# Optimization experiments

Hardware: AMD Instinct MI355X
Metric: run time of the kernel (lower is better)

Reference implementation:

```python
import jax, jax.numpy as jnp
import numpy as np

B, S, E = 4, 2048, 1024
H = 16
D = E // H  # head_dim = 64


def setup_inputs() -> dict:
    key = jax.random.key(0)
    ks = jax.random.split(key, 7)
    query = jax.random.normal(ks[0], (B, S, E), dtype=jnp.float32)
    k_in = jax.random.normal(ks[1], (B, S, E), dtype=jnp.float32)
    v_in = jax.random.normal(ks[2], (B, S, E), dtype=jnp.float32)
    lim_qkv = 1.0 / np.sqrt(E)
    W_qkv = jax.random.uniform(ks[3], (E, 3 * E), jnp.float32, -lim_qkv, lim_qkv)
    b_qkv = jax.random.uniform(ks[4], (3 * E,), jnp.float32, -lim_qkv, lim_qkv)
    W_out = jax.random.uniform(ks[5], (E, E), jnp.float32, -lim_qkv, lim_qkv)
    b_out = jax.random.uniform(ks[6], (E,), jnp.float32, -lim_qkv, lim_qkv)
    return {"query": query, "key": k_in, "value": v_in,
            "W_qkv": W_qkv, "b_qkv": b_qkv, "W_out": W_out, "b_out": b_out}


def reference(query, key, value, W_qkv, b_qkv, W_out, b_out):
    # NOTE: original module ignores key/value; q,k,v all derived from query.
    b, s, e = query.shape
    qkv = query @ W_qkv + b_qkv                     # [B,S,3E]
    qkv = qkv.reshape(b, s, 3, H, D)
    q, k, v = qkv[:, :, 0], qkv[:, :, 1], qkv[:, :, 2]   # [B,S,H,D]
    scale = jnp.sqrt(jnp.asarray(D, dtype=jnp.float32))
    scores = jnp.einsum('bqhd,bkhd->bhqk', q, k) / scale  # [B,H,S,S]
    attn = jax.nn.softmax(scores, axis=-1)
    out = jnp.einsum('bhqk,bkhd->bqhd', attn, v).reshape(b, s, e)
    return out @ W_out + b_out
```

## Files before the change

### kernel.cpp

```cpp
#include <hip/hip_runtime.h>
#include <hip/hip_bf16.h>

#define Bc 4
#define Sc 2048
#define Ec 1024
#define Hc 16
#define Dc 64

typedef __bf16 bf16_t;
typedef __bf16 bf16x8 __attribute__((ext_vector_type(8)));
typedef float f32x4 __attribute__((ext_vector_type(4)));

extern "C" __device__ float __ocml_native_exp2_f32(float);

__device__ __forceinline__ f32x4 mfma16(bf16x8 a, bf16x8 b, f32x4 c) {
    return __builtin_amdgcn_mfma_f32_16x16x32_bf16(a, b, c, 0, 0, 0);
}

__device__ __forceinline__ void gload16(const bf16_t* g, bf16_t* l) {
    __builtin_amdgcn_global_load_lds(
        (const __attribute__((address_space(1))) unsigned int*)g,
        (__attribute__((address_space(3))) unsigned int*)l, 16, 0, 0);
}

__global__ __launch_bounds__(256)
void cvt_bf16(const float* __restrict__ in, bf16_t* __restrict__ out, int n4)
{
    int i = blockIdx.x * 256 + threadIdx.x;
    if (i >= n4) return;
    float4 v = ((const float4*)in)[i];
    alignas(8) bf16_t o[4];
    o[0] = (bf16_t)v.x; o[1] = (bf16_t)v.y; o[2] = (bf16_t)v.z; o[3] = (bf16_t)v.w;
    ((uint2*)out)[i] = *(uint2*)o;
}

__global__ __launch_bounds__(256)
void transpose_w(const float* __restrict__ W, bf16_t* __restrict__ Wt, int K, int N)
{
    __shared__ float T[64][65];
    const int kt = blockIdx.y, nt = blockIdx.x;
    const int r = threadIdx.x >> 4;
    const int c = (threadIdx.x & 15) * 4;
    #pragma unroll
    for (int p = 0; p < 4; p++) {
        float4 v = *(const float4*)(W + (size_t)(kt*64 + r + p*16)*N + nt*64 + c);
        T[r + p*16][c] = v.x; T[r + p*16][c+1] = v.y;
        T[r + p*16][c+2] = v.z; T[r + p*16][c+3] = v.w;
    }
    __syncthreads();
    #pragma unroll
    for (int p = 0; p < 4; p++) {
        int n = nt*64 + r + p*16;
        alignas(8) bf16_t tmp[4];
        #pragma unroll
        for (int j = 0; j < 4; j++) tmp[j] = (bf16_t)T[c + j][r + p*16];
        *(uint2*)(Wt + (size_t)n*K + kt*64 + c) = *(uint2*)tmp;
    }
}

__global__ __launch_bounds__(256)
void transpose_v(const bf16_t* __restrict__ qkv, bf16_t* __restrict__ vt)
{
    __shared__ bf16_t T[64][72];
    const int bh = blockIdx.y, st = blockIdx.x;
    const int b = bh >> 4, h = bh & 15;
    const int sr = threadIdx.x >> 3;
    const int dc = (threadIdx.x & 7) * 8;
    #pragma unroll
    for (int p = 0; p < 2; p++) {
        const bf16_t* src = qkv + (size_t)(b*Sc + st*64 + sr + p*32)*(3*Ec) + 2*Ec + h*Dc + dc;
        *(uint4*)&T[sr + p*32][dc] = *(const uint4*)src;
    }
    __syncthreads();
    const int dr = threadIdx.x >> 3;
    const int sc2 = (threadIdx.x & 7) * 8;
    #pragma unroll
    for (int p = 0; p < 2; p++) {
        alignas(16) bf16_t tmp[8];
        #pragma unroll
        for (int j = 0; j < 8; j++) {
            int q = sc2 + j;
            int o = ((q & 3) << 4) | (q >> 2);
            tmp[j] = T[o][dr + p*32];
        }
        *(uint4*)(vt + (size_t)bh*Dc*Sc + (size_t)(dr + p*32)*Sc + st*64 + sc2) = *(uint4*)tmp;
    }
}

template<int OUT_IS_F32>
__global__ __launch_bounds__(256)
void gemm_bt(const bf16_t* __restrict__ A, const bf16_t* __restrict__ Bt,
             const float* __restrict__ biasp, void* __restrict__ Cp,
             int M, int N, int K)
{
    __shared__ bf16_t As[2][128*32];
    __shared__ bf16_t Bs[2][128*32];

    const int tid  = threadIdx.x;
    const int wave = tid >> 6;
    const int lane = tid & 63;
    const int quad = lane >> 4;
    const int l16  = lane & 15;
    const int wm   = (wave >> 1) * 64;
    const int wn   = (wave & 1) * 64;
    const int m0   = blockIdx.y * 128;
    const int n0   = blockIdx.x * 128;

    const int srow = wave*32 + (lane >> 2);
    const int scol = (lane & 3) * 8;
    const bf16_t* ap0 = A  + (size_t)(m0 + srow)      * K + scol;
    const bf16_t* ap1 = A  + (size_t)(m0 + srow + 16) * K + scol;
    const bf16_t* bp0 = Bt + (size_t)(n0 + srow)      * K + scol;
    const bf16_t* bp1 = Bt + (size_t)(n0 + srow + 16) * K + scol;
    bf16_t* asl0 = &As[0][(wave*32)      * 32];
    bf16_t* asl1 = &As[0][(wave*32 + 16) * 32];
    bf16_t* bsl0 = &Bs[0][(wave*32)      * 32];
    bf16_t* bsl1 = &Bs[0][(wave*32 + 16) * 32];
    bf16_t* asl2 = &As[1][(wave*32)      * 32];
    bf16_t* asl3 = &As[1][(wave*32 + 16) * 32];
    bf16_t* bsl2 = &Bs[1][(wave*32)      * 32];
    bf16_t* bsl3 = &Bs[1][(wave*32 + 16) * 32];

    f32x4 acc[4][4] = {};

    for (int k0 = 0; k0 < K; k0 += 64) {
        gload16(ap0 + k0,      asl0);
        gload16(ap1 + k0,      asl1);
        gload16(ap0 + k0 + 32, asl2);
        gload16(ap1 + k0 + 32, asl3);
        gload16(bp0 + k0,      bsl0);
        gload16(bp1 + k0,      bsl1);
        gload16(bp0 + k0 + 32, bsl2);
        gload16(bp1 + k0 + 32, bsl3);
        __syncthreads();

        #pragma unroll
        for (int kc = 0; kc < 2; kc++) {
            bf16x8 af[4], bfr[4];
            #pragma unroll
            for (int mi = 0; mi < 4; mi++)
                af[mi] = *(const bf16x8*)&As[kc][(wm + mi*16 + l16)*32 + quad*8];
            #pragma unroll
            for (int ni = 0; ni < 4; ni++)
                bfr[ni] = *(const bf16x8*)&Bs[kc][(wn + ni*16 + l16)*32 + quad*8];
            #pragma unroll
            for (int mi = 0; mi < 4; mi++)
                #pragma unroll
                for (int ni = 0; ni < 4; ni++)
                    acc[mi][ni] = mfma16(af[mi], bfr[ni], acc[mi][ni]);
        }
        __syncthreads();
    }

    float bv[4];
    #pragma unroll
    for (int ni = 0; ni < 4; ni++) bv[ni] = biasp[n0 + wn + ni*16 + l16];

    #pragma unroll
    for (int mi = 0; mi < 4; mi++)
        #pragma unroll
        for (int ni = 0; ni < 4; ni++)
            #pragma unroll
            for (int r = 0; r < 4; r++) {
                int row = m0 + wm + mi*16 + quad*4 + r;
                int col = n0 + wn + ni*16 + l16;
                float v = acc[mi][ni][r] + bv[ni];
                if (OUT_IS_F32) ((float*)Cp)[(size_t)row * N + col] = v;
                else            ((bf16_t*)Cp)[(size_t)row * N + col] = (bf16_t)v;
            }
}

__global__ __launch_bounds__(256, 2)
void attn5(const bf16_t* __restrict__ qkv, const bf16_t* __restrict__ vt,
           bf16_t* __restrict__ aout)
{
    __shared__ bf16_t Ks[64][72];
    __shared__ bf16_t Vs[64][72];
    __shared__ bf16_t Ps[4][64][72];

    const int tid  = threadIdx.x;
    const int wave = tid >> 6;
    const int lane = tid & 63;
    const int quad = lane >> 4;
    const int l16  = lane & 15;
    const int bh   = blockIdx.y;
    const int b    = bh >> 4;
    const int h    = bh & 15;
    const int qt   = blockIdx.x;
    const float kscale = 0.125f * 1.44269504088896340736f;

    bf16x8 qf[4][2];
    #pragma unroll
    for (int mi = 0; mi < 4; mi++) {
        const bf16_t* qrow = qkv + (size_t)(b*Sc + qt*256 + wave*64 + mi*16 + l16)*(3*Ec) + h*Dc;
        qf[mi][0] = *(const bf16x8*)(qrow + quad*8);
        qf[mi][1] = *(const bf16x8*)(qrow + 32 + quad*8);
        #pragma unroll
        for (int f = 0; f < 2; f++)
            #pragma unroll
            for (int e = 0; e < 8; e++)
                qf[mi][f][e] = (bf16_t)((float)qf[mi][f][e] * kscale);
    }

    bf16x8 ones;
    #pragma unroll
    for (int e = 0; e < 8; e++) ones[e] = (bf16_t)1.0f;

    f32x4 acc[4][4] = {};
    f32x4 acc_l[4] = {};

    const int krw   = tid >> 2;
    const int dbase = (tid & 3) * 16;

    const bf16_t* kbase = qkv + (size_t)(b*Sc + krw)*(3*Ec) + Ec + h*Dc + dbase;
    const bf16_t* vbase = vt + (size_t)bh*Dc*Sc + (size_t)krw*Sc + dbase;
    const size_t kstep = (size_t)64 * (3*Ec);
    uint4 ku0 = ((const uint4*)kbase)[0];
    uint4 ku1 = ((const uint4*)kbase)[1];
    uint4 vu0 = ((const uint4*)vbase)[0];
    uint4 vu1 = ((const uint4*)vbase)[1];

    for (int kt = 0; kt < Sc/64; kt++) {
        __syncthreads();
        *(uint4*)&Ks[krw][dbase]     = ku0;
        *(uint4*)&Ks[krw][dbase + 8] = ku1;
        *(uint4*)&Vs[krw][dbase]     = vu0;
        *(uint4*)&Vs[krw][dbase + 8] = vu1;
        __syncthreads();

        if (kt < Sc/64 - 1) {
            const bf16_t* kn = kbase + (size_t)(kt+1) * kstep;
            const bf16_t* vn = vbase + (kt+1) * 64;
            ku0 = ((const uint4*)kn)[0];
            ku1 = ((const uint4*)kn)[1];
            vu0 = ((const uint4*)vn)[0];
            vu1 = ((const uint4*)vn)[1];
        }

        bf16x8 kf[4][2];
        #pragma unroll
        for (int ni = 0; ni < 4; ni++) {
            kf[ni][0] = *(const bf16x8*)&Ks[ni*16 + l16][quad*8];
            kf[ni][1] = *(const bf16x8*)&Ks[ni*16 + l16][32 + quad*8];
        }

        #pragma unroll
        for (int mi = 0; mi < 4; mi++) {
            f32x4 sf[4];
            #pragma unroll
            for (int ni = 0; ni < 4; ni++) {
                f32x4 z = {};
                z = mfma16(qf[mi][0], kf[ni][0], z);
                z = mfma16(qf[mi][1], kf[ni][1], z);
                sf[ni] = z;
            }
            #pragma unroll
            for (int rr = 0; rr < 4; rr++) {
                float p0 = __ocml_native_exp2_f32(sf[0][rr]);
                float p1 = __ocml_native_exp2_f32(sf[1][rr]);
                float p2 = __ocml_native_exp2_f32(sf[2][rr]);
                float p3 = __ocml_native_exp2_f32(sf[3][rr]);
                alignas(8) bf16_t pw[4];
                pw[0] = (bf16_t)p0; pw[1] = (bf16_t)p1;
                pw[2] = (bf16_t)p2; pw[3] = (bf16_t)p3;
                *(uint2*)&Ps[wave][mi*16 + quad*4 + rr][4*l16] = *(uint2*)pw;
            }
        }

        asm volatile("s_waitcnt lgkmcnt(0)" ::: "memory");

        bf16x8 pf[4][2];
        #pragma unroll
        for (int mi = 0; mi < 4; mi++) {
            pf[mi][0] = *(const bf16x8*)&Ps[wave][mi*16 + l16][quad*8];
            pf[mi][1] = *(const bf16x8*)&Ps[wave][mi*16 + l16][32 + quad*8];
        }
        #pragma unroll
        for (int mi = 0; mi < 4; mi++) {
            acc_l[mi] = mfma16(pf[mi][0], ones, acc_l[mi]);
            acc_l[mi] = mfma16(pf[mi][1], ones, acc_l[mi]);
        }
        #pragma unroll
        for (int ni = 0; ni < 4; ni++) {
            bf16x8 v0 = *(const bf16x8*)&Vs[ni*16 + l16][quad*8];
            bf16x8 v1 = *(const bf16x8*)&Vs[ni*16 + l16][32 + quad*8];
            #pragma unroll
            for (int mi = 0; mi < 4; mi++) {
                acc[mi][ni] = mfma16(pf[mi][0], v0, acc[mi][ni]);
                acc[mi][ni] = mfma16(pf[mi][1], v1, acc[mi][ni]);
            }
        }
    }

    #pragma unroll
    for (int mi = 0; mi < 4; mi++)
        #pragma unroll
        for (int rr = 0; rr < 4; rr++) {
            float inv = 1.0f / acc_l[mi][rr];
            int row = qt*256 + wave*64 + mi*16 + quad*4 + rr;
            #pragma unroll
            for (int ni = 0; ni < 4; ni++) {
                int col = h*Dc + ni*16 + l16;
                aout[(size_t)(b*Sc + row)*Ec + col] = (bf16_t)(acc[mi][ni][rr] * inv);
            }
        }
}

extern "C" void kernel_launch(void* const* d_in, const int* in_sizes, int n_in,
                              void* d_out, int out_size, void* d_ws, size_t ws_size,
                              hipStream_t stream) {
    const float* query = (const float*)d_in[0];
    const float* W_qkv = (const float*)d_in[3];
    const float* b_qkv = (const float*)d_in[4];
    const float* W_out = (const float*)d_in[5];
    const float* b_out = (const float*)d_in[6];
    float* out = (float*)d_out;

    const size_t MT = (size_t)Bc * Sc;
    char* ws = (char*)d_ws;
    bf16_t* qbf     = (bf16_t*)ws;
    bf16_t* qkv_ws  = (bf16_t*)(ws + MT*Ec*2);
    bf16_t* vt_ws   = (bf16_t*)(ws + MT*Ec*2 + MT*3*Ec*2);
    bf16_t* wqkv_t  = (bf16_t*)(ws + MT*Ec*2 + MT*3*Ec*2 + MT*Ec*2);
    bf16_t* wout_t  = (bf16_t*)(ws + MT*Ec*2 + MT*3*Ec*2 + MT*Ec*2 + (size_t)3*Ec*Ec*2);

    cvt_bf16<<<(MT*Ec/4 + 255)/256, 256, 0, stream>>>(query, qbf, (int)(MT*Ec/4));
    transpose_w<<<dim3(3*Ec/64, Ec/64), 256, 0, stream>>>(W_qkv, wqkv_t, Ec, 3*Ec);
    transpose_w<<<dim3(Ec/64, Ec/64), 256, 0, stream>>>(W_out, wout_t, Ec, Ec);

    gemm_bt<0><<<dim3(3*Ec/128, MT/128), 256, 0, stream>>>(
        qbf, wqkv_t, b_qkv, qkv_ws, (int)MT, 3*Ec, Ec);

    transpose_v<<<dim3(Sc/64, Bc*Hc), 256, 0, stream>>>(qkv_ws, vt_ws);

    attn5<<<dim3(Sc/256, Bc*Hc), 256, 0, stream>>>(qkv_ws, vt_ws, qbf);

    gemm_bt<1><<<dim3(Ec/128, MT/128), 256, 0, stream>>>(
        qbf, wout_t, b_out, out, (int)MT, Ec, Ec);
}
```

Before: 321.4 us.

## Keep softmax probabilities in registers by computing transposed S and O tiles

The attention kernel now computes S^T = K·Q^T so the MFMA output layout of the exp'd scores matches the B-operand layout for the P·V product. This removes the per-wave LDS staging buffer for P and the extra MFMAs that summed row totals against a ones vector. Row sums are accumulated in registers and combined with cross-lane shuffles at the end. Because the output is produced transposed, it is written to a new workspace buffer and a separate transpose kernel restores the [B,S,E] layout, which adds a launch and extra memory traffic. Freeing the LDS lets the launch bound allow three blocks per SM instead of two.

```diff
diff --git a/kernel.cpp b/kernel.cpp
--- a/kernel.cpp
+++ b/kernel.cpp
@@ -8,6 +8,7 @@
 #define Dc 64
 
 typedef __bf16 bf16_t;
+typedef __bf16 bf16x4 __attribute__((ext_vector_type(4)));
 typedef __bf16 bf16x8 __attribute__((ext_vector_type(8)));
 typedef float f32x4 __attribute__((ext_vector_type(4)));
 
@@ -78,12 +79,35 @@
     for (int p = 0; p < 2; p++) {
         alignas(16) bf16_t tmp[8];
         #pragma unroll
-        for (int j = 0; j < 8; j++) {
-            int q = sc2 + j;
-            int o = ((q & 3) << 4) | (q >> 2);
-            tmp[j] = T[o][dr + p*32];
-        }
+        for (int j = 0; j < 8; j++)
+            tmp[j] = T[sc2 + j][dr + p*32];
         *(uint4*)(vt + (size_t)bh*Dc*Sc + (size_t)(dr + p*32)*Sc + st*64 + sc2) = *(uint4*)tmp;
+    }
+}
+
+__global__ __launch_bounds__(256)
+void otransp(const bf16_t* __restrict__ ot, bf16_t* __restrict__ attn)
+{
+    __shared__ bf16_t T[64][72];
+    const int bh = blockIdx.y, st = blockIdx.x;
+    const int b = bh >> 4, h = bh & 15;
+    const int dr = threadIdx.x >> 3;
+    const int sc = (threadIdx.x & 7) * 8;
+    #pragma unroll
+    for (int p = 0; p < 2; p++) {
+        const bf16_t* src = ot + ((size_t)bh*Dc + dr + p*32)*Sc + st*64 + sc;
+        *(uint4*)&T[dr + p*32][sc] = *(const uint4*)src;
+    }
+    __syncthreads();
+    const int sr = threadIdx.x >> 3;
+    const int dc = (threadIdx.x & 7) * 8;
+    #pragma unroll
+    for (int p = 0; p < 2; p++) {
+        alignas(16) bf16_t tmp[8];
+        #pragma unroll
+        for (int j = 0; j < 8; j++)
+            tmp[j] = T[dc + j][sr + p*32];
+        *(uint4*)(attn + (size_t)(b*Sc + st*64 + sr + p*32)*Ec + h*Dc + dc) = *(uint4*)tmp;
     }
 }
 
@@ -170,13 +194,12 @@
             }
 }
 
-__global__ __launch_bounds__(256, 2)
-void attn5(const bf16_t* __restrict__ qkv, const bf16_t* __restrict__ vt,
-           bf16_t* __restrict__ aout)
+__global__ __launch_bounds__(256, 3)
+void attn6(const bf16_t* __restrict__ qkv, const bf16_t* __restrict__ vt,
+           bf16_t* __restrict__ ot)
 {
     __shared__ bf16_t Ks[64][72];
     __shared__ bf16_t Vs[64][72];
-    __shared__ bf16_t Ps[4][64][72];
 
     const int tid  = threadIdx.x;
     const int wave = tid >> 6;
@@ -191,23 +214,19 @@
 
     bf16x8 qf[4][2];
     #pragma unroll
-    for (int mi = 0; mi < 4; mi++) {
-        const bf16_t* qrow = qkv + (size_t)(b*Sc + qt*256 + wave*64 + mi*16 + l16)*(3*Ec) + h*Dc;
-        qf[mi][0] = *(const bf16x8*)(qrow + quad*8);
-        qf[mi][1] = *(const bf16x8*)(qrow + 32 + quad*8);
+    for (int qi = 0; qi < 4; qi++) {
+        const bf16_t* qrow = qkv + (size_t)(b*Sc + qt*256 + wave*64 + qi*16 + l16)*(3*Ec) + h*Dc;
+        qf[qi][0] = *(const bf16x8*)(qrow + quad*8);
+        qf[qi][1] = *(const bf16x8*)(qrow + 32 + quad*8);
         #pragma unroll
         for (int f = 0; f < 2; f++)
             #pragma unroll
             for (int e = 0; e < 8; e++)
-                qf[mi][f][e] = (bf16_t)((float)qf[mi][f][e] * kscale);
-    }
-
-    bf16x8 ones;
-    #pragma unroll
-    for (int e = 0; e < 8; e++) ones[e] = (bf16_t)1.0f;
+                qf[qi][f][e] = (bf16_t)((float)qf[qi][f][e] * kscale);
+    }
 
     f32x4 acc[4][4] = {};
-    f32x4 acc_l[4] = {};
+    float lpart[4] = {};
 
     const int krw   = tid >> 2;
     const int dbase = (tid & 3) * 16;
@@ -239,69 +258,67 @@
 
         bf16x8 kf[4][2];
         #pragma unroll
-        for (int ni = 0; ni < 4; ni++) {
-            kf[ni][0] = *(const bf16x8*)&Ks[ni*16 + l16][quad*8];
-            kf[ni][1] = *(const bf16x8*)&Ks[ni*16 + l16][32 + quad*8];
-        }
-
-        #pragma unroll
-        for (int mi = 0; mi < 4; mi++) {
-            f32x4 sf[4];
-            #pragma unroll
-            for (int ni = 0; ni < 4; ni++) {
+        for (int ki = 0; ki < 4; ki++) {
+            kf[ki][0] = *(const bf16x8*)&Ks[ki*16 + l16][quad*8];
+            kf[ki][1] = *(const bf16x8*)&Ks[ki*16 + l16][32 + quad*8];
+        }
+
+        bf16x4 pp[4][4];
+        #pragma unroll
+        for (int ki = 0; ki < 4; ki++) {
+            #pragma unroll
+            for (int qi = 0; qi < 4; qi++) {
                 f32x4 z = {};
-                z = mfma16(qf[mi][0], kf[ni][0], z);
-                z = mfma16(qf[mi][1], kf[ni][1], z);
-                sf[ni] = z;
+                z = mfma16(kf[ki][0], qf[qi][0], z);
+                z = mfma16(kf[ki][1], qf[qi][1], z);
+                float p0 = __ocml_native_exp2_f32(z[0]);
+                float p1 = __ocml_native_exp2_f32(z[1]);
+                float p2 = __ocml_native_exp2_f32(z[2]);
+                float p3 = __ocml_native_exp2_f32(z[3]);
+                lpart[qi] += (p0 + p1) + (p2 + p3);
+                bf16x4 w;
+                w[0] = (bf16_t)p0; w[1] = (bf16_t)p1;
+                w[2] = (bf16_t)p2; w[3] = (bf16_t)p3;
+                pp[ki][qi] = w;
             }
-            #pragma unroll
-            for (int rr = 0; rr < 4; rr++) {
-                float p0 = __ocml_native_exp2_f32(sf[0][rr]);
-                float p1 = __ocml_native_exp2_f32(sf[1][rr]);
-                float p2 = __ocml_native_exp2_f32(sf[2][rr]);
-                float p3 = __ocml_native_exp2_f32(sf[3][rr]);
-                alignas(8) bf16_t pw[4];
-                pw[0] = (bf16_t)p0; pw[1] = (bf16_t)p1;
-                pw[2] = (bf16_t)p2; pw[3] = (bf16_t)p3;
-                *(uint2*)&Ps[wave][mi*16 + quad*4 + rr][4*l16] = *(uint2*)pw;
+        }
+
+        #pragma unroll
+        for (int c = 0; c < 2; c++) {
+            bf16x8 pcat[4];
+            #pragma unroll
+            for (int qi = 0; qi < 4; qi++)
+                pcat[qi] = __builtin_shufflevector(pp[2*c][qi], pp[2*c+1][qi],
+                                                   0,1,2,3,4,5,6,7);
+            #pragma unroll
+            for (int di = 0; di < 4; di++) {
+                bf16x4 v0 = *(const bf16x4*)&Vs[di*16 + l16][c*32 + 4*quad];
+                bf16x4 v1 = *(const bf16x4*)&Vs[di*16 + l16][c*32 + 16 + 4*quad];
+                bf16x8 vf = __builtin_shufflevector(v0, v1, 0,1,2,3,4,5,6,7);
+                #pragma unroll
+                for (int qi = 0; qi < 4; qi++)
+                    acc[di][qi] = mfma16(vf, pcat[qi], acc[di][qi]);
             }
         }
-
-        asm volatile("s_waitcnt lgkmcnt(0)" ::: "memory");
-
-        bf16x8 pf[4][2];
-        #pragma unroll
-        for (int mi = 0; mi < 4; mi++) {
-            pf[mi][0] = *(const bf16x8*)&Ps[wave][mi*16 + l16][quad*8];
-            pf[mi][1] = *(const bf16x8*)&Ps[wave][mi*16 + l16][32 + quad*8];
-        }
-        #pragma unroll
-        for (int mi = 0; mi < 4; mi++) {
-            acc_l[mi] = mfma16(pf[mi][0], ones, acc_l[mi]);
-            acc_l[mi] = mfma16(pf[mi][1], ones, acc_l[mi]);
-        }
-        #pragma unroll
-        for (int ni = 0; ni < 4; ni++) {
-            bf16x8 v0 = *(const bf16x8*)&Vs[ni*16 + l16][quad*8];
-            bf16x8 v1 = *(const bf16x8*)&Vs[ni*16 + l16][32 + quad*8];
-            #pragma unroll
-            for (int mi = 0; mi < 4; mi++) {
-                acc[mi][ni] = mfma16(pf[mi][0], v0, acc[mi][ni]);
-                acc[mi][ni] = mfma16(pf[mi][1], v1, acc[mi][ni]);
-            }
-        }
-    }
-
-    #pragma unroll
-    for (int mi = 0; mi < 4; mi++)
-        #pragma unroll
-        for (int rr = 0; rr < 4; rr++) {
-            float inv = 1.0f / acc_l[mi][rr];
-            int row = qt*256 + wave*64 + mi*16 + quad*4 + rr;
-            #pragma unroll
-            for (int ni = 0; ni < 4; ni++) {
-                int col = h*Dc + ni*16 + l16;
-                aout[(size_t)(b*Sc + row)*Ec + col] = (bf16_t)(acc[mi][ni][rr] * inv);
+    }
+
+    float inv[4];
+    #pragma unroll
+    for (int qi = 0; qi < 4; qi++) {
+        float l = lpart[qi];
+        l += __shfl_xor(l, 16);
+        l += __shfl_xor(l, 32);
+        inv[qi] = 1.0f / l;
+    }
+    #pragma unroll
+    for (int di = 0; di < 4; di++)
+        #pragma unroll
+        for (int qi = 0; qi < 4; qi++) {
+            int qg = qt*256 + wave*64 + qi*16 + l16;
+            #pragma unroll
+            for (int r = 0; r < 4; r++) {
+                int d = di*16 + quad*4 + r;
+                ot[((size_t)bh*Dc + d)*Sc + qg] = (bf16_t)(acc[di][qi][r] * inv[qi]);
             }
         }
 }
@@ -318,11 +335,13 @@
 
     const size_t MT = (size_t)Bc * Sc;
     char* ws = (char*)d_ws;
-    bf16_t* qbf     = (bf16_t*)ws;
-    bf16_t* qkv_ws  = (bf16_t*)(ws + MT*Ec*2);
-    bf16_t* vt_ws   = (bf16_t*)(ws + MT*Ec*2 + MT*3*Ec*2);
-    bf16_t* wqkv_t  = (bf16_t*)(ws + MT*Ec*2 + MT*3*Ec*2 + MT*Ec*2);
-    bf16_t* wout_t  = (bf16_t*)(ws + MT*Ec*2 + MT*3*Ec*2 + MT*Ec*2 + (size_t)3*Ec*Ec*2);
+    size_t off = 0;
+    bf16_t* qbf    = (bf16_t*)(ws + off); off += MT*Ec*2;
+    bf16_t* qkv_ws = (bf16_t*)(ws + off); off += MT*3*Ec*2;
+    bf16_t* vt_ws  = (bf16_t*)(ws + off); off += MT*Ec*2;
+    bf16_t* wqkv_t = (bf16_t*)(ws + off); off += (size_t)3*Ec*Ec*2;
+    bf16_t* wout_t = (bf16_t*)(ws + off); off += (size_t)Ec*Ec*2;
+    bf16_t* ot_ws  = (bf16_t*)(ws + off); off += MT*Ec*2;
 
     cvt_bf16<<<(MT*Ec/4 + 255)/256, 256, 0, stream>>>(query, qbf, (int)(MT*Ec/4));
     transpose_w<<<dim3(3*Ec/64, Ec/64), 256, 0, stream>>>(W_qkv, wqkv_t, Ec, 3*Ec);
@@ -333,7 +352,9 @@
 
     transpose_v<<<dim3(Sc/64, Bc*Hc), 256, 0, stream>>>(qkv_ws, vt_ws);
 
-    attn5<<<dim3(Sc/256, Bc*Hc), 256, 0, stream>>>(qkv_ws, vt_ws, qbf);
+    attn6<<<dim3(Sc/256, Bc*Hc), 256, 0, stream>>>(qkv_ws, vt_ws, ot_ws);
+
+    otransp<<<dim3(Sc/64, Bc*Hc), 256, 0, stream>>>(ot_ws, qbf);
 
     gemm_bt<1><<<dim3(Ec/128, MT/128), 256, 0, stream>>>(
         qbf, wout_t, b_out, out, (int)MT, Ec, Ec);
```

Result: slower. 449.5 us (+39.8%).
